# Kernel tuning notes

Hardware: AMD Instinct MI355X
Metric: run time of the kernel (lower is better)

Reference implementation:

```python
import jax, jax.numpy as jnp
import numpy as np

PEP_LEN = 15
IN_CH = 512
OUT_CH = 512
BATCH = 8192


def setup_inputs() -> dict:
    key = jax.random.key(0)
    k_x, k_w = jax.random.split(key)
    peptide_x = jax.random.normal(k_x, (BATCH, PEP_LEN, IN_CH), dtype=jnp.float32)
    # truncated_normal_(std=0.02) init; plain normal*0.02 is fine for a numeric reference
    weight = jax.random.normal(k_w, (PEP_LEN, IN_CH, OUT_CH), dtype=jnp.float32) * 0.02
    bias = jnp.zeros((PEP_LEN, OUT_CH), dtype=jnp.float32)
    return {"peptide_x": peptide_x, "weight": weight, "bias": bias}


def reference(peptide_x, weight, bias) -> jnp.ndarray:
    # Original torch code does a full tensordot over all pep_len positions
    # ([B,P,P,O]) then gathers the diagonal. That is mathematically identical
    # to a per-position batched matmul, which we compute directly.
    out = jnp.einsum('bpi,pio->bpo', peptide_x, weight)  # [B, P, O]
    return out + bias  # bias broadcasts over batch
```

## Files before the change

kernel.cpp:

```cpp
#include <hip/hip_runtime.h>
#include <hip/hip_bf16.h>
#include <stdint.h>

#define BATCH 8192
#define PEP 15
#define INC 512
#define OUTC 512
#define XROW (PEP*INC)
#define WT_P_ELEMS (INC*OUTC)
#define NSTEPS 16

typedef float f32x4 __attribute__((ext_vector_type(4)));
typedef short s16x8 __attribute__((ext_vector_type(8)));
typedef unsigned int u32x4 __attribute__((ext_vector_type(4)));

__device__ __forceinline__ ushort f2b(float v) {
  uint u = __float_as_uint(v);
  u += 0x7fffu + ((u >> 16) & 1u);
  return (ushort)(u >> 16);
}

__device__ __forceinline__ uint cvtpk(float a, float b) {
  uint r;
  asm("v_cvt_pk_bf16_f32 %0, %1, %2" : "=v"(r) : "v"(a), "v"(b));
  return r;
}

__global__ __launch_bounds__(256) void wt_kernel(const float* __restrict__ w,
                                                 ushort* __restrict__ wt) {
  int gid = blockIdx.x * 256 + threadIdx.x;
  int l   = gid & 63;
  int n16 = (gid >> 6) & 31;
  int ks  = (gid >> 11) & 15;
  int p   = gid >> 15;
  int fr = l & 15, g = l >> 4;
  const float* src = w + (size_t)p * WT_P_ELEMS + (size_t)(ks * 32 + g * 8) * OUTC + n16 * 16 + fr;
  s16x8 hv;
#pragma unroll
  for (int e = 0; e < 8; ++e) hv[e] = (short)f2b(src[(size_t)e * OUTC]);
  *(s16x8*)(wt + (size_t)gid * 8) = hv;
}

__global__ __launch_bounds__(512, 4) void gemm_kernel(const float* __restrict__ x,
                                                      const ushort* __restrict__ wt,
                                                      const float* __restrict__ bias,
                                                      float* __restrict__ out) {
  __shared__ __align__(16) char lds_raw[49152];
  typedef ushort AshT[8][64][8];
  typedef ushort BshT[16][64][8];
  AshT* Ash = (AshT*)lds_raw;
  BshT* Bsh = (BshT*)(lds_raw + 16384);

  const int t    = threadIdx.x;
  const int lane = t & 63;
  const int wid  = t >> 6;
  const int wm   = wid >> 2;
  const int wn   = wid & 3;
  const int fr   = lane & 15;
  const int g    = lane >> 4;

  const int bid  = blockIdx.x;
  const int xcd  = bid & 7;
  const int j    = bid >> 3;
  const int n2   = j & 1;
  const int pair = xcd * 120 + (j >> 1);
  const int mb   = pair & 63;
  const int p    = pair >> 6;
  const int m0   = mb * 128;

  const float* asrc = x + (size_t)(m0 + wid * 16 + fr) * XROW + p * INC + g * 8;

  const ushort* bsrc = wt + (size_t)p * WT_P_ELEMS
                     + (size_t)(n2 * 16 + wid * 2) * 512 + (size_t)lane * 8;

  f32x4 acc[4][4] = {};
  f32x4 pa0, pa1;

  auto cvt_store = [&](int buf) {
    u32x4 aw;
    aw[0] = cvtpk(pa0[0], pa0[1]); aw[1] = cvtpk(pa0[2], pa0[3]);
    aw[2] = cvtpk(pa1[0], pa1[1]); aw[3] = cvtpk(pa1[2], pa1[3]);
    *(u32x4*)&Ash[buf][wid][lane][0] = aw;
  };
  auto stageB = [&](int ks, int buf) {
#pragma unroll
    for (int q = 0; q < 2; ++q) {
      __builtin_amdgcn_global_load_lds(
          (const __attribute__((address_space(1))) void*)(bsrc + (size_t)ks * 16384 + q * 512),
          (__attribute__((address_space(3))) void*)(&Bsh[buf][wid * 2 + q][lane][0]),
          16, 0, 0);
    }
  };

  pa0 = *(const f32x4*)(asrc);
  pa1 = *(const f32x4*)(asrc + 4);
  cvt_store(0);
  stageB(0, 0);
  pa0 = *(const f32x4*)(asrc + 32);
  pa1 = *(const f32x4*)(asrc + 36);
  __syncthreads();

#pragma unroll
  for (int ks = 0; ks < NSTEPS; ++ks) {
    const int cur = ks & 1;
    const int nxt = cur ^ 1;

    if (ks + 1 < NSTEPS) {
      cvt_store(nxt);
      stageB(ks + 1, nxt);
    }
    if (ks + 2 < NSTEPS) {
      pa0 = *(const f32x4*)(asrc + (ks + 2) * 32);
      pa1 = *(const f32x4*)(asrc + (ks + 2) * 32 + 4);
    }

    s16x8 af[4];
#pragma unroll
    for (int i = 0; i < 4; ++i)
      af[i] = *(const s16x8*)&Ash[cur][wm * 4 + i][lane][0];

    s16x8 bf[4];
#pragma unroll
    for (int nf = 0; nf < 4; ++nf)
      bf[nf] = *(const s16x8*)&Bsh[cur][wn * 4 + nf][lane][0];

#pragma unroll
    for (int i = 0; i < 4; ++i)
#pragma unroll
      for (int nf = 0; nf < 4; ++nf)
        acc[i][nf] = __builtin_amdgcn_mfma_f32_16x16x32_bf16(af[i], bf[nf], acc[i][nf], 0, 0, 0);

    __syncthreads();
  }

  const int n0 = n2 * 256 + wn * 64;
  float bv[4];
#pragma unroll
  for (int nf = 0; nf < 4; ++nf) bv[nf] = bias[p * OUTC + n0 + nf * 16 + fr];

  float* trans = (float*)(lds_raw + wid * 4352);
  const int er = lane >> 4;
  const int ec = (lane & 15) * 4;

#pragma unroll
  for (int m16 = 0; m16 < 4; ++m16) {
    __builtin_amdgcn_sched_barrier(0);
#pragma unroll
    for (int nf = 0; nf < 4; ++nf)
#pragma unroll
      for (int r = 0; r < 4; ++r)
        trans[(g * 4 + r) * 68 + nf * 16 + fr] = acc[m16][nf][r] + bv[nf];
    __builtin_amdgcn_sched_barrier(0);
    asm volatile("s_waitcnt lgkmcnt(0)" ::: "memory");
    __builtin_amdgcn_sched_barrier(0);
    float* ob = out + (size_t)(m0 + wm * 64 + m16 * 16) * XROW + p * INC + n0;
#pragma unroll
    for (int pass = 0; pass < 4; ++pass) {
      const int row = pass * 4 + er;
      f32x4 v = *(const f32x4*)&trans[row * 68 + ec];
      __builtin_nontemporal_store(v, (f32x4*)(ob + (size_t)row * XROW + ec));
    }
    __builtin_amdgcn_sched_barrier(0);
    asm volatile("s_waitcnt lgkmcnt(0)" ::: "memory");
    __builtin_amdgcn_sched_barrier(0);
  }
}

__global__ void naive_kernel(const float* __restrict__ x, const float* __restrict__ w,
                             const float* __restrict__ bias, float* __restrict__ out) {
  size_t i = (size_t)blockIdx.x * 256 + threadIdx.x;
  if (i >= (size_t)BATCH * PEP * OUTC) return;
  int o  = (int)(i & (OUTC - 1));
  int pp = (int)((i >> 9) % PEP);
  size_t b = i / ((size_t)PEP * OUTC);
  const float* xr = x + b * XROW + pp * INC;
  const float* wc = w + (size_t)pp * INC * OUTC + o;
  float s = bias[pp * OUTC + o];
  for (int k = 0; k < INC; ++k) s += xr[k] * wc[(size_t)k * OUTC];
  out[i] = s;
}

extern "C" void kernel_launch(void* const* d_in, const int* in_sizes, int n_in,
                              void* d_out, int out_size, void* d_ws, size_t ws_size,
                              hipStream_t stream) {
  const float* x    = (const float*)d_in[0];
  const float* w    = (const float*)d_in[1];
  const float* bias = (const float*)d_in[2];
  float* out = (float*)d_out;

  const size_t wt_bytes = (size_t)PEP * INC * OUTC * sizeof(ushort);
  if (ws_size >= wt_bytes) {
    wt_kernel<<<1920, 256, 0, stream>>>(w, (ushort*)d_ws);
    gemm_kernel<<<1920, 512, 0, stream>>>(x, (const ushort*)d_ws, bias, out);
  } else {
    size_t total = (size_t)BATCH * PEP * OUTC;
    naive_kernel<<<(int)((total + 255) / 256), 256, 0, stream>>>(x, w, bias, out);
  }
}
```

Baseline: 149.5 us.

## Enlarge GEMM tile to 256 rows and 64-wide K steps with 1024-thread blocks

Doubles the per-block M tile to 256 rows and the K step to 64 by running 16 waves per block. Each step now loads two 32-wide K sub-slices of A and B into 128 KB of dynamic LDS, which halves the number of K iterations and barriers. The grid shrinks from 1920 to 960 blocks, and each weight tile is reused across more rows. In exchange, the larger LDS footprint likely allows only one block per CU, so fewer waves are resident to hide latency on this memory-heavy kernel. The launcher also raises the kernel's dynamic shared memory limit and falls back to the naive kernel if that call fails.

```diff
diff --git a/kernel.cpp b/kernel.cpp
--- a/kernel.cpp
+++ b/kernel.cpp
@@ -8,7 +8,7 @@
 #define OUTC 512
 #define XROW (PEP*INC)
 #define WT_P_ELEMS (INC*OUTC)
-#define NSTEPS 16
+#define NSTEPS 8
 
 typedef float f32x4 __attribute__((ext_vector_type(4)));
 typedef short s16x8 __attribute__((ext_vector_type(8)));
@@ -41,15 +41,13 @@
   *(s16x8*)(wt + (size_t)gid * 8) = hv;
 }
 
-__global__ __launch_bounds__(512, 4) void gemm_kernel(const float* __restrict__ x,
-                                                      const ushort* __restrict__ wt,
-                                                      const float* __restrict__ bias,
-                                                      float* __restrict__ out) {
-  __shared__ __align__(16) char lds_raw[49152];
-  typedef ushort AshT[8][64][8];
-  typedef ushort BshT[16][64][8];
-  AshT* Ash = (AshT*)lds_raw;
-  BshT* Bsh = (BshT*)(lds_raw + 16384);
+__global__ __launch_bounds__(1024, 4) void gemm_kernel(const float* __restrict__ x,
+                                                       const ushort* __restrict__ wt,
+                                                       const float* __restrict__ bias,
+                                                       float* __restrict__ out) {
+  extern __shared__ __align__(16) char lds_raw[];
+  auto Ash = (ushort (*)[16][2][64][8])lds_raw;
+  auto Bsh = (ushort (*)[2][16][64][8])(lds_raw + 65536);
 
   const int t    = threadIdx.x;
   const int lane = t & 63;
@@ -63,41 +61,52 @@
   const int xcd  = bid & 7;
   const int j    = bid >> 3;
   const int n2   = j & 1;
-  const int pair = xcd * 120 + (j >> 1);
-  const int mb   = pair & 63;
-  const int p    = pair >> 6;
-  const int m0   = mb * 128;
+  const int pair = xcd * 60 + (j >> 1);
+  const int mb   = pair & 31;
+  const int p    = pair >> 5;
+  const int m0   = mb * 256;
 
   const float* asrc = x + (size_t)(m0 + wid * 16 + fr) * XROW + p * INC + g * 8;
 
-  const ushort* bsrc = wt + (size_t)p * WT_P_ELEMS
-                     + (size_t)(n2 * 16 + wid * 2) * 512 + (size_t)lane * 8;
+  const ushort* wt_p = wt + (size_t)p * WT_P_ELEMS + (size_t)lane * 8;
 
   f32x4 acc[4][4] = {};
-  f32x4 pa0, pa1;
-
+  f32x4 pa[2][2];
+
+  auto load_pa = [&](int ks) {
+#pragma unroll
+    for (int ksub = 0; ksub < 2; ++ksub) {
+      pa[ksub][0] = *(const f32x4*)(asrc + ks * 64 + ksub * 32);
+      pa[ksub][1] = *(const f32x4*)(asrc + ks * 64 + ksub * 32 + 4);
+    }
+  };
   auto cvt_store = [&](int buf) {
-    u32x4 aw;
-    aw[0] = cvtpk(pa0[0], pa0[1]); aw[1] = cvtpk(pa0[2], pa0[3]);
-    aw[2] = cvtpk(pa1[0], pa1[1]); aw[3] = cvtpk(pa1[2], pa1[3]);
-    *(u32x4*)&Ash[buf][wid][lane][0] = aw;
+#pragma unroll
+    for (int ksub = 0; ksub < 2; ++ksub) {
+      u32x4 aw;
+      aw[0] = cvtpk(pa[ksub][0][0], pa[ksub][0][1]); aw[1] = cvtpk(pa[ksub][0][2], pa[ksub][0][3]);
+      aw[2] = cvtpk(pa[ksub][1][0], pa[ksub][1][1]); aw[3] = cvtpk(pa[ksub][1][2], pa[ksub][1][3]);
+      *(u32x4*)&Ash[buf][wid][ksub][lane][0] = aw;
+    }
   };
   auto stageB = [&](int ks, int buf) {
 #pragma unroll
     for (int q = 0; q < 2; ++q) {
+      const int c    = wid * 2 + q;
+      const int ksb  = c >> 4;
+      const int n16l = c & 15;
       __builtin_amdgcn_global_load_lds(
-          (const __attribute__((address_space(1))) void*)(bsrc + (size_t)ks * 16384 + q * 512),
-          (__attribute__((address_space(3))) void*)(&Bsh[buf][wid * 2 + q][lane][0]),
+          (const __attribute__((address_space(1))) void*)
+            (wt_p + ((size_t)(ks * 2 + ksb) * 32 + n2 * 16 + n16l) * 512),
+          (__attribute__((address_space(3))) void*)(&Bsh[buf][ksb][n16l][lane][0]),
           16, 0, 0);
     }
   };
 
-  pa0 = *(const f32x4*)(asrc);
-  pa1 = *(const f32x4*)(asrc + 4);
+  load_pa(0);
   cvt_store(0);
   stageB(0, 0);
-  pa0 = *(const f32x4*)(asrc + 32);
-  pa1 = *(const f32x4*)(asrc + 36);
+  load_pa(1);
   __syncthreads();
 
 #pragma unroll
@@ -109,26 +118,23 @@
       cvt_store(nxt);
       stageB(ks + 1, nxt);
     }
-    if (ks + 2 < NSTEPS) {
-      pa0 = *(const f32x4*)(asrc + (ks + 2) * 32);
-      pa1 = *(const f32x4*)(asrc + (ks + 2) * 32 + 4);
-    }
-
-    s16x8 af[4];
-#pragma unroll
-    for (int i = 0; i < 4; ++i)
-      af[i] = *(const s16x8*)&Ash[cur][wm * 4 + i][lane][0];
-
-    s16x8 bf[4];
-#pragma unroll
-    for (int nf = 0; nf < 4; ++nf)
-      bf[nf] = *(const s16x8*)&Bsh[cur][wn * 4 + nf][lane][0];
-
-#pragma unroll
-    for (int i = 0; i < 4; ++i)
+    if (ks + 2 < NSTEPS) load_pa(ks + 2);
+
+#pragma unroll
+    for (int ksub = 0; ksub < 2; ++ksub) {
+      s16x8 af[4], bf[4];
+#pragma unroll
+      for (int i = 0; i < 4; ++i)
+        af[i] = *(const s16x8*)&Ash[cur][wm * 4 + i][ksub][lane][0];
 #pragma unroll
       for (int nf = 0; nf < 4; ++nf)
-        acc[i][nf] = __builtin_amdgcn_mfma_f32_16x16x32_bf16(af[i], bf[nf], acc[i][nf], 0, 0, 0);
+        bf[nf] = *(const s16x8*)&Bsh[cur][ksub][wn * 4 + nf][lane][0];
+#pragma unroll
+      for (int i = 0; i < 4; ++i)
+#pragma unroll
+        for (int nf = 0; nf < 4; ++nf)
+          acc[i][nf] = __builtin_amdgcn_mfma_f32_16x16x32_bf16(af[i], bf[nf], acc[i][nf], 0, 0, 0);
+    }
 
     __syncthreads();
   }
@@ -189,9 +195,15 @@
   float* out = (float*)d_out;
 
   const size_t wt_bytes = (size_t)PEP * INC * OUTC * sizeof(ushort);
-  if (ws_size >= wt_bytes) {
+  static int lds_ok = -1;
+  if (lds_ok < 0) {
+    hipError_t e = hipFuncSetAttribute(reinterpret_cast<const void*>(gemm_kernel),
+                                       hipFuncAttributeMaxDynamicSharedMemorySize, 131072);
+    lds_ok = (e == hipSuccess) ? 1 : 0;
+  }
+  if (ws_size >= wt_bytes && lds_ok == 1) {
     wt_kernel<<<1920, 256, 0, stream>>>(w, (ushort*)d_ws);
-    gemm_kernel<<<1920, 512, 0, stream>>>(x, (const ushort*)d_ws, bias, out);
+    gemm_kernel<<<960, 1024, 131072, stream>>>(x, (const ushort*)d_ws, bias, out);
   } else {
     size_t total = (size_t)BATCH * PEP * OUTC;
     naive_kernel<<<(int)((total + 255) / 256), 256, 0, stream>>>(x, w, bias, out);
```

After: 165.9 us. 1.11x slower.
